# Optimization experiments

Measured on AMD Instinct MI355X. Metric: run time of the kernel, lower is better.

The kernel has to match this reference:

```python
import jax, jax.numpy as jnp
import numpy as np

B, N, H, W, C = 512, 16, 84, 84, 3
CNN_OUT, ATTN, GH, HEADS, POS, A_DIM = 256, 64, 128, 2, 3, 3
IN_GAT = CNN_OUT + POS  # 259
FLAT = 64 * 16 * 16     # conv output flat dim for 84x84 input


def setup_inputs() -> dict:
    key = jax.random.key(0)
    ks = jax.random.split(key, 16)
    s = 0.05
    return dict(
        cam=jax.random.uniform(ks[0], (B, H, W, C), jnp.float32),
        pos=jax.random.normal(ks[1], (B, POS), jnp.float32),
        team_pos=jax.random.normal(ks[2], (B, N, POS), jnp.float32) * 10.0,
        agent_idx=jax.random.randint(ks[3], (B,), 0, N),
        W1=jax.random.normal(ks[4], (32, C, 8, 8), jnp.float32) * s, b1=jnp.zeros((32,), jnp.float32),
        W2=jax.random.normal(ks[5], (64, 32, 4, 4), jnp.float32) * s, b2=jnp.zeros((64,), jnp.float32),
        W3=jax.random.normal(ks[6], (64, 64, 3, 3), jnp.float32) * s, b3=jnp.zeros((64,), jnp.float32),
        Wp=jax.random.normal(ks[7], (FLAT, CNN_OUT), jnp.float32) * 0.01, bp=jnp.zeros((CNN_OUT,), jnp.float32),
        Wid=jax.random.normal(ks[8], (1, ATTN), jnp.float32) * s, bid=jnp.zeros((ATTN,), jnp.float32),
        Wg=jax.random.normal(ks[9], (IN_GAT, HEADS * GH), jnp.float32) * s,
        a_src=jax.random.normal(ks[10], (HEADS, GH), jnp.float32) * s,
        a_dst=jax.random.normal(ks[11], (HEADS, GH), jnp.float32) * s,
        Wh1=jax.random.normal(ks[12], (HEADS * GH + ATTN, 256), jnp.float32) * s, bh1=jnp.zeros((256,), jnp.float32),
        Wh2=jax.random.normal(ks[13], (256, 2 * A_DIM), jnp.float32) * s, bh2=jnp.zeros((2 * A_DIM,), jnp.float32),
    )


def _conv(x, w, b, stride):
    y = jax.lax.conv_general_dilated(x, w, (stride, stride), 'VALID',
                                     dimension_numbers=('NCHW', 'OIHW', 'NCHW'))
    return jax.nn.relu(y + b[None, :, None, None])


def reference(cam, pos, team_pos, agent_idx, W1, b1, W2, b2, W3, b3, Wp, bp,
              Wid, bid, Wg, a_src, a_dst, Wh1, bh1, Wh2, bh2):
    # CNN encoder (NHWC -> NCHW)
    x = jnp.transpose(cam, (0, 3, 1, 2))
    x = _conv(x, W1, b1, 2)   # [B,32,39,39]
    x = _conv(x, W2, b2, 2)   # [B,64,18,18]
    x = _conv(x, W3, b3, 1)   # [B,64,16,16]
    cam_feat = jax.nn.relu(x.reshape(x.shape[0], -1) @ Wp + bp)  # [B,256]

    # per-node features: broadcast ego cam feat + relative team positions
    rel_pos = team_pos - pos[:, None, :]                                     # [B,N,3]
    node_feats = jnp.concatenate(
        [jnp.broadcast_to(cam_feat[:, None, :], (B, N, CNN_OUT)), rel_pos], axis=-1)  # [B,N,259]

    # adjacency: within 100m, no self-loops, self-loop added for isolated nodes
    dist = jnp.linalg.norm(team_pos[:, :, None, :] - team_pos[:, None, :, :], axis=-1)  # [B,N,N]
    eye = jnp.eye(N, dtype=node_feats.dtype)
    adj = (dist < 100.0).astype(node_feats.dtype) * (1.0 - eye)
    need_self = (adj.sum(axis=2) == 0).astype(adj.dtype)                     # [B,N]
    adj = adj + eye[None] * need_self[..., None]

    # dense multi-head GAT layer
    hN = (node_feats @ Wg).reshape(B, N, HEADS, GH)                          # [B,N,H,D]
    src = jnp.einsum('bnhd,hd->bnh', hN, a_src)
    dst = jnp.einsum('bnhd,hd->bnh', hN, a_dst)
    e = jax.nn.leaky_relu(src[:, :, None, :] + dst[:, None, :, :], 0.2)      # [B,i,j,H]
    e = jnp.where(adj[..., None] > 0, e, -1e9)
    alpha = jax.nn.softmax(e, axis=2)
    h = jnp.einsum('bijh,bjhd->bihd', alpha, hN).reshape(B, N, HEADS * GH)   # [B,N,256]
    h = jax.nn.elu(h)
    h = jnp.nan_to_num(h, nan=0.0, posinf=0.0, neginf=0.0)

    # agent-id embedding, fuse, gather own node, policy head
    id_emb = jax.nn.relu(agent_idx.astype(jnp.float32)[:, None] @ Wid + bid)  # [B,64]
    fused = jnp.concatenate([h, jnp.broadcast_to(id_emb[:, None, :], (B, N, ATTN))], axis=-1)  # [B,N,320]
    agent_feat = fused[jnp.arange(B), agent_idx]                             # [B,320]
    z = jax.nn.relu(agent_feat @ Wh1 + bh1)
    logits = z @ Wh2 + bh2                                                    # [B,6]
    return logits
```

## Files before the change

### kernel.cpp

```cpp
#include <hip/hip_runtime.h>


typedef __attribute__((ext_vector_type(8))) short bf16x8;
typedef __attribute__((ext_vector_type(4))) float f32x4;

union U4 { uint4 v; unsigned int u[4]; bf16x8 h; };

__device__ __forceinline__ unsigned short f2bf(float x) {
    unsigned int u = __float_as_uint(x);
    return (unsigned short)((u + 0x7FFFu + ((u >> 16) & 1u)) >> 16);
}
__device__ __forceinline__ unsigned int pack2(float lo, float hi) {
    return (unsigned int)f2bf(lo) | ((unsigned int)f2bf(hi) << 16);
}
__device__ __forceinline__ bf16x8 loadA(const unsigned int* __restrict__ W, int k8, int M, int oc) {
    U4 r; r.v = *(const uint4*)(W + (((size_t)k8 * M + oc) << 2));
    return r.h;
}
__device__ __forceinline__ bf16x8 loadB4(const unsigned int* __restrict__ base, size_t idx) {
    U4 r; r.v = *(const uint4*)(base + (idx << 2));
    return r.h;
}
__device__ __forceinline__ bf16x8 loadBp(const unsigned int* __restrict__ p, size_t BC) {
    U4 r; r.u[0] = p[0]; r.u[1] = p[BC]; r.u[2] = p[2 * BC]; r.u[3] = p[3 * BC];
    return r.h;
}
#define MFMA(a, b, c) __builtin_amdgcn_mfma_f32_16x16x32_bf16((a), (b), (c), 0, 0, 0)

__device__ __forceinline__ int xcd_swz(int L, int nwg) {
    int q = nwg >> 3, r = nwg & 7;
    int x = L & 7, i = L >> 3;
    return (x < r ? x * (q + 1) : r * (q + 1) + (x - r) * q) + i;
}

__device__ __forceinline__ void storeK(unsigned int* __restrict__ out,
                                       size_t row, size_t BC, size_t bcol,
                                       int lg, unsigned int u0, unsigned int u1) {
    uint2 v; v.x = u0; v.y = u1;
    *(uint2*)(out + ((row * BC + bcol) << 2) + ((lg & 1) << 1)) = v;
}

__global__ __launch_bounds__(256) void prepack(
    const float* __restrict__ W1, const float* __restrict__ W2,
    const float* __restrict__ W3, const float* __restrict__ Wp,
    const float* __restrict__ Wg, const float* __restrict__ Wh1,
    unsigned int* __restrict__ W1t, unsigned int* __restrict__ W2t,
    unsigned int* __restrict__ W3t, unsigned int* __restrict__ Wpt,
    unsigned int* __restrict__ Wgt, unsigned int* __restrict__ Wh1t)
{
    int i = blockIdx.x * 256 + threadIdx.x;
    if (i < 3072) {
        int j2 = i & 3, oc = (i >> 2) & 31, k8 = i >> 7;
        int c = k8 >> 3, kh = k8 & 7, kw = 2 * j2;
        const float* s = W1 + ((oc * 3 + c) * 8 + kh) * 8;
        W1t[i] = pack2(s[kw], s[kw + 1]);
    } else if (i < 19456) {
        int j = i - 3072;
        int j2 = j & 3, oc = (j >> 2) & 63, k8 = j >> 8;
        int tap = k8 >> 2, ic = (k8 & 3) * 8 + 2 * j2;
        int kh = tap >> 2, kw = tap & 3;
        float a = W2[((oc * 32 + ic) * 4 + kh) * 4 + kw];
        float b = W2[((oc * 32 + ic + 1) * 4 + kh) * 4 + kw];
        W2t[j] = pack2(a, b);
    } else if (i < 37888) {
        int j = i - 19456;
        int j2 = j & 3, oc = (j >> 2) & 63, k8 = j >> 8;
        int tap = k8 >> 3, ic = (k8 & 7) * 8 + 2 * j2;
        int kh = tap / 3, kw = tap % 3;
        float a = W3[((oc * 64 + ic) * 3 + kh) * 3 + kw];
        float b = W3[((oc * 64 + ic + 1) * 3 + kh) * 3 + kw];
        W3t[j] = pack2(a, b);
    } else if (i < 2135040) {
        int j = i - 37888;
        int j2 = j & 3, n = (j >> 2) & 255, k8 = j >> 10;
        int s3 = k8 >> 3, oc = (k8 & 7) * 8 + 2 * j2;
        float a = Wp[(size_t)(oc * 256 + s3) * 256 + n];
        float b = Wp[(size_t)((oc + 1) * 256 + s3) * 256 + n];
        Wpt[j] = pack2(a, b);
    } else if (i < 2167808) {
        int j = i - 2135040;
        int j2 = j & 3, m = (j >> 2) & 255, k8 = j >> 10;
        int k = k8 * 8 + 2 * j2;
        Wgt[j] = pack2(Wg[k * 256 + m], Wg[(k + 1) * 256 + m]);
    } else if (i < 2208768) {
        int j = i - 2167808;
        int j2 = j & 3, m = (j >> 2) & 255, k8 = j >> 10;
        int k = k8 * 8 + 2 * j2;
        Wh1t[j] = pack2(Wh1[k * 256 + m], Wh1[(k + 1) * 256 + m]);
    }
}

__global__ __launch_bounds__(256) void transpose_cam(
    const float* __restrict__ cam, unsigned int* __restrict__ camt, int b0, int BC)
{
    __shared__ float lds[32][253];
    int yy = blockIdx.x;
    int bb = blockIdx.y * 32;
    int t = threadIdx.x;
    for (int f = t; f < 8064; f += 256) {
        int b = f / 252, p = f - b * 252;
        lds[b][p] = cam[(size_t)(b0 + bb + b) * 21168 + yy * 252 + p];
    }
    __syncthreads();
    for (int g = t; g < 4032; g += 256) {
        int b = g & 31, q = g >> 5;
        int c = q / 42, x2 = q - c * 42;
        unsigned int v = pack2(lds[b][6 * x2 + c], lds[b][6 * x2 + 3 + c]);
        camt[(size_t)((c * 84 + yy) * 42 + x2) * BC + bb + b] = v;
    }
}

__global__ __launch_bounds__(256) void conv1_mfma(
    const unsigned int* __restrict__ in32, const unsigned int* __restrict__ Wt,
    const float* __restrict__ bias, unsigned int* __restrict__ out32,
    int BC, int nspat)
{
    int wgid = xcd_swz(blockIdx.x, gridDim.x);
    int s = wgid % nspat;
    int bq = wgid / nspat;
    int oh = s / 39, ow = s - oh * 39;
    int wv = threadIdx.x >> 6, l = threadIdx.x & 63;
    int lg = l >> 4, lc = l & 15;
    const size_t sBC = (size_t)BC;
    size_t base = (size_t)bq * 256 + wv * 64 + lc;
    f32x4 acc[2][4] = {};
    int ybase = 2 * oh;
    #pragma unroll
    for (int sp = 0; sp < 3; sp++) {
        const int s0 = 2 * sp, s1 = s0 + 1;
        bf16x8 A0[2], A1[2], B0[4], B1[4];
        #pragma unroll
        for (int m = 0; m < 2; m++) {
            A0[m] = loadA(Wt, s0 * 4 + lg, 32, m * 16 + lc);
            A1[m] = loadA(Wt, s1 * 4 + lg, 32, m * 16 + lc);
        }
        const unsigned int* p0 = in32 + (size_t)((sp * 84 + ybase + lg) * 42 + ow) * sBC + base;
        const unsigned int* p1 = in32 + (size_t)((sp * 84 + ybase + 4 + lg) * 42 + ow) * sBC + base;
        #pragma unroll
        for (int g = 0; g < 4; g++) {
            B0[g] = loadBp(p0 + g * 16, sBC);
            B1[g] = loadBp(p1 + g * 16, sBC);
        }
        #pragma unroll
        for (int m = 0; m < 2; m++)
            #pragma unroll
            for (int g = 0; g < 4; g++)
                acc[m][g] = MFMA(A0[m], B0[g], acc[m][g]);
        #pragma unroll
        for (int m = 0; m < 2; m++)
            #pragma unroll
            for (int g = 0; g < 4; g++)
                acc[m][g] = MFMA(A1[m], B1[g], acc[m][g]);
    }
    #pragma unroll
    for (int m = 0; m < 2; m++) {
        float4 bv = *(const float4*)(bias + m * 16 + lg * 4);
        size_t row = (size_t)s * 4 + 2 * m + (lg >> 1);
        #pragma unroll
        for (int g = 0; g < 4; g++) {
            f32x4 a = acc[m][g];
            unsigned int u0 = pack2(fmaxf(a.x + bv.x, 0.f), fmaxf(a.y + bv.y, 0.f));
            unsigned int u1 = pack2(fmaxf(a.z + bv.z, 0.f), fmaxf(a.w + bv.w, 0.f));
            storeK(out32, row, sBC, base + g * 16, lg, u0, u1);
        }
    }
}

__global__ __launch_bounds__(256) void conv2_mfma(
    const unsigned int* __restrict__ in32, const unsigned int* __restrict__ Wt,
    const float* __restrict__ bias, unsigned int* __restrict__ out32,
    int BC, int nspat)
{
    int wgid = xcd_swz(blockIdx.x, gridDim.x);
    int s = wgid % nspat;
    int bq = wgid / nspat;
    int oh = s / 18, ow = s - oh * 18;
    int wv = threadIdx.x >> 6, l = threadIdx.x & 63;
    int lg = l >> 4, lc = l & 15;
    const size_t sBC = (size_t)BC;
    size_t base = (size_t)bq * 256 + wv * 64 + lc;
    f32x4 acc[4][4] = {};
    int ybase = 2 * oh, xbase = 2 * ow;
    #pragma unroll
    for (int sp = 0; sp < 8; sp++) {
        const int s0 = 2 * sp, s1 = s0 + 1;
        bf16x8 A0[4], A1[4], B0[4], B1[4];
        #pragma unroll
        for (int m = 0; m < 4; m++) {
            A0[m] = loadA(Wt, s0 * 4 + lg, 64, m * 16 + lc);
            A1[m] = loadA(Wt, s1 * 4 + lg, 64, m * 16 + lc);
        }
        {
            const int kh = s0 >> 2, kw = s0 & 3;
            size_t row = (size_t)(((ybase + kh) * 39 + xbase + kw) * 4 + lg);
            #pragma unroll
            for (int g = 0; g < 4; g++)
                B0[g] = loadB4(in32, row * sBC + base + g * 16);
        }
        {
            const int kh = s1 >> 2, kw = s1 & 3;
            size_t row = (size_t)(((ybase + kh) * 39 + xbase + kw) * 4 + lg);
            #pragma unroll
            for (int g = 0; g < 4; g++)
                B1[g] = loadB4(in32, row * sBC + base + g * 16);
        }
        #pragma unroll
        for (int m = 0; m < 4; m++)
            #pragma unroll
            for (int g = 0; g < 4; g++)
                acc[m][g] = MFMA(A0[m], B0[g], acc[m][g]);
        #pragma unroll
        for (int m = 0; m < 4; m++)
            #pragma unroll
            for (int g = 0; g < 4; g++)
                acc[m][g] = MFMA(A1[m], B1[g], acc[m][g]);
    }
    #pragma unroll
    for (int m = 0; m < 4; m++) {
        float4 bv = *(const float4*)(bias + m * 16 + lg * 4);
        size_t row = (size_t)s * 8 + 2 * m + (lg >> 1);
        #pragma unroll
        for (int g = 0; g < 4; g++) {
            f32x4 a = acc[m][g];
            unsigned int u0 = pack2(fmaxf(a.x + bv.x, 0.f), fmaxf(a.y + bv.y, 0.f));
            unsigned int u1 = pack2(fmaxf(a.z + bv.z, 0.f), fmaxf(a.w + bv.w, 0.f));
            storeK(out32, row, sBC, base + g * 16, lg, u0, u1);
        }
    }
}

__global__ __launch_bounds__(256) void conv3_mfma(
    const unsigned int* __restrict__ in32, const unsigned int* __restrict__ Wt,
    const float* __restrict__ bias, unsigned int* __restrict__ out32,
    int BC, int nspat)
{
    int wgid = xcd_swz(blockIdx.x, gridDim.x);
    int s = wgid % nspat;
    int bq = wgid / nspat;
    int oh = s >> 4, ow = s & 15;
    int wv = threadIdx.x >> 6, l = threadIdx.x & 63;
    int lg = l >> 4, lc = l & 15;
    const size_t sBC = (size_t)BC;
    size_t base = (size_t)bq * 256 + wv * 64 + lc;
    f32x4 acc[4][4] = {};
    #pragma unroll
    for (int sp = 0; sp < 9; sp++) {
        const int s0 = 2 * sp, s1 = s0 + 1;
        const int kh = sp / 3, kw = sp - kh * 3;
        bf16x8 A0[4], A1[4], B0[4], B1[4];
        #pragma unroll
        for (int m = 0; m < 4; m++) {
            A0[m] = loadA(Wt, s0 * 4 + lg, 64, m * 16 + lc);
            A1[m] = loadA(Wt, s1 * 4 + lg, 64, m * 16 + lc);
        }
        size_t row0 = (size_t)(((oh + kh) * 18 + ow + kw) * 8 + lg);
        #pragma unroll
        for (int g = 0; g < 4; g++) {
            B0[g] = loadB4(in32, row0 * sBC + base + g * 16);
            B1[g] = loadB4(in32, (row0 + 4) * sBC + base + g * 16);
        }
        #pragma unroll
        for (int m = 0; m < 4; m++)
            #pragma unroll
            for (int g = 0; g < 4; g++)
                acc[m][g] = MFMA(A0[m], B0[g], acc[m][g]);
        #pragma unroll
        for (int m = 0; m < 4; m++)
            #pragma unroll
            for (int g = 0; g < 4; g++)
                acc[m][g] = MFMA(A1[m], B1[g], acc[m][g]);
    }
    #pragma unroll
    for (int m = 0; m < 4; m++) {
        float4 bv = *(const float4*)(bias + m * 16 + lg * 4);
        size_t row = (size_t)s * 8 + 2 * m + (lg >> 1);
        #pragma unroll
        for (int g = 0; g < 4; g++) {
            f32x4 a = acc[m][g];
            unsigned int u0 = pack2(fmaxf(a.x + bv.x, 0.f), fmaxf(a.y + bv.y, 0.f));
            unsigned int u1 = pack2(fmaxf(a.z + bv.z, 0.f), fmaxf(a.w + bv.w, 0.f));
            storeK(out32, row, sBC, base + g * 16, lg, u0, u1);
        }
    }
}

__global__ __launch_bounds__(256) void proj_mfma(
    const unsigned int* __restrict__ x3, const unsigned int* __restrict__ Wpt,
    float* __restrict__ partial, int BC)
{
    int wgid = xcd_swz(blockIdx.x, gridDim.x);
    int rem = wgid & 127;
    int bq = wgid >> 7;
    int mq = rem & 3;
    int kseg = rem >> 2;
    int wv = threadIdx.x >> 6, l = threadIdx.x & 63;
    int lg = l >> 4, lc = l & 15;
    const size_t sBC = (size_t)BC;
    size_t base = (size_t)bq * 256 + wv * 64 + lc;
    f32x4 acc[4][4] = {};
    #pragma unroll
    for (int sp = 0; sp < 8; sp++) {
        const int k8b = kseg * 64 + sp * 8;
        bf16x8 A0[4], A1[4], B0[4], B1[4];
        #pragma unroll
        for (int m = 0; m < 4; m++) {
            A0[m] = loadA(Wpt, k8b + lg, 256, mq * 64 + m * 16 + lc);
            A1[m] = loadA(Wpt, k8b + 4 + lg, 256, mq * 64 + m * 16 + lc);
        }
        #pragma unroll
        for (int g = 0; g < 4; g++) {
            B0[g] = loadB4(x3, (size_t)(k8b + lg) * sBC + base + g * 16);
            B1[g] = loadB4(x3, (size_t)(k8b + 4 + lg) * sBC + base + g * 16);
        }
        #pragma unroll
        for (int m = 0; m < 4; m++)
            #pragma unroll
            for (int g = 0; g < 4; g++)
                acc[m][g] = MFMA(A0[m], B0[g], acc[m][g]);
        #pragma unroll
        for (int m = 0; m < 4; m++)
            #pragma unroll
            for (int g = 0; g < 4; g++)
                acc[m][g] = MFMA(A1[m], B1[g], acc[m][g]);
    }
    #pragma unroll
    for (int m = 0; m < 4; m++) {
        size_t row4 = (size_t)kseg * 64 + mq * 16 + m * 4 + lg;
        #pragma unroll
        for (int g = 0; g < 4; g++)
            *(f32x4*)(partial + ((row4 * sBC + base + g * 16) << 2)) = acc[m][g];
    }
}

__global__ __launch_bounds__(256) void reduce_k(
    const float* __restrict__ partial, const float* __restrict__ bp,
    unsigned int* __restrict__ cf16, int b0, int BC, int bcShift)
{
    int i = blockIdx.x * 256 + threadIdx.x;
    int bl = i & (BC - 1);
    int k8 = i >> bcShift;
    f32x4 S0 = {}, S1 = {};
    for (int seg = 0; seg < 32; seg++) {
        const float* p = partial + (((size_t)(seg * 64 + k8 * 2) * BC + bl) << 2);
        S0 += *(const f32x4*)p;
        S1 += *(const f32x4*)(p + (BC << 2));
    }
    int n = k8 * 8;
    uint4 u;
    u.x = pack2(fmaxf(S0.x + bp[n + 0], 0.f), fmaxf(S0.y + bp[n + 1], 0.f));
    u.y = pack2(fmaxf(S0.z + bp[n + 2], 0.f), fmaxf(S0.w + bp[n + 3], 0.f));
    u.z = pack2(fmaxf(S1.x + bp[n + 4], 0.f), fmaxf(S1.y + bp[n + 5], 0.f));
    u.w = pack2(fmaxf(S1.z + bp[n + 6], 0.f), fmaxf(S1.w + bp[n + 7], 0.f));
    *(uint4*)(cf16 + (((size_t)k8 * 512 + b0 + bl) << 2)) = u;
}

__global__ __launch_bounds__(64) void gat_prep(
    const unsigned int* __restrict__ cf16, const unsigned int* __restrict__ Wgt,
    float* __restrict__ hNb)
{
    int mq = blockIdx.x, bq = blockIdx.y;
    int l = threadIdx.x, lg = l >> 4, lc = l & 15;
    size_t bcol = (size_t)bq * 32 + lc;
    f32x4 acc[4][2] = {};
    #pragma unroll
    for (int sp = 0; sp < 4; sp++) {
        const int s0 = 2 * sp, s1 = s0 + 1;
        bf16x8 A0[4], A1[4], B0[2], B1[2];
        #pragma unroll
        for (int m = 0; m < 4; m++) {
            A0[m] = loadA(Wgt, s0 * 4 + lg, 256, mq * 64 + m * 16 + lc);
            A1[m] = loadA(Wgt, s1 * 4 + lg, 256, mq * 64 + m * 16 + lc);
        }
        #pragma unroll
        for (int g = 0; g < 2; g++) {
            B0[g] = loadB4(cf16, (size_t)(s0 * 4 + lg) * 512 + bcol + g * 16);
            B1[g] = loadB4(cf16, (size_t)(s1 * 4 + lg) * 512 + bcol + g * 16);
        }
        #pragma unroll
        for (int m = 0; m < 4; m++) {
            acc[m][0] = MFMA(A0[m], B0[0], acc[m][0]);
            acc[m][1] = MFMA(A0[m], B0[1], acc[m][1]);
            acc[m][0] = MFMA(A1[m], B1[0], acc[m][0]);
            acc[m][1] = MFMA(A1[m], B1[1], acc[m][1]);
        }
    }
    #pragma unroll
    for (int m = 0; m < 4; m++) {
        #pragma unroll
        for (int g = 0; g < 2; g++) {
            size_t b = (size_t)bq * 32 + g * 16 + lc;
            int row0 = mq * 64 + m * 16 + lg * 4;
            *(f32x4*)(hNb + b * 256 + row0) = acc[m][g];
        }
    }
}

__global__ __launch_bounds__(256) void gat_mid(
    const float* __restrict__ hNb, const float* __restrict__ pos,
    const float* __restrict__ tpos, const int* __restrict__ aidx,
    const float* __restrict__ Wg, const float* __restrict__ asrc, const float* __restrict__ adst,
    const float* __restrict__ Wid, const float* __restrict__ bid,
    unsigned int* __restrict__ af16)
{
    int b = blockIdx.x, t = threadIdx.x;
    __shared__ float hN[16][256];
    __shared__ float srcv[16][2], dstv[16][2];
    __shared__ float alpha[16][2];
    __shared__ float af[320];
    __shared__ unsigned int adjm_s;

    int ai = aidx[b];
    float basev = hNb[(size_t)b * 256 + t];
    float rw0 = Wg[65536 + t], rw1 = Wg[65792 + t], rw2 = Wg[66048 + t];
    float px = pos[b * 3 + 0], py = pos[b * 3 + 1], pz = pos[b * 3 + 2];
    for (int n = 0; n < 16; n++) {
        float r0 = tpos[(b * 16 + n) * 3 + 0] - px;
        float r1 = tpos[(b * 16 + n) * 3 + 1] - py;
        float r2 = tpos[(b * 16 + n) * 3 + 2] - pz;
        hN[n][t] = basev + r0 * rw0 + r1 * rw1 + r2 * rw2;
    }

    if (t < 64) {
        bool on = false;
        if (t < 16 && t != ai) {
            float dx = tpos[(b * 16 + ai) * 3 + 0] - tpos[(b * 16 + t) * 3 + 0];
            float dy = tpos[(b * 16 + ai) * 3 + 1] - tpos[(b * 16 + t) * 3 + 1];
            float dz = tpos[(b * 16 + ai) * 3 + 2] - tpos[(b * 16 + t) * 3 + 2];
            on = (dx * dx + dy * dy + dz * dz) < 10000.0f;
        }
        unsigned long long m = __ballot(on);
        if (t == 0) adjm_s = (m == 0ull) ? (1u << ai) : (unsigned int)m;
    }
    __syncthreads();

    {
        int p = t >> 3, sub = t & 7;
        int j = p >> 1, h = p & 1;
        float s1 = 0.f, s2 = 0.f;
        #pragma unroll
        for (int dd = 0; dd < 16; dd++) {
            int d = h * 128 + sub * 16 + dd;
            float v = hN[j][d];
            s1 += v * asrc[d];
            s2 += v * adst[d];
        }
        s1 += __shfl_xor(s1, 1); s1 += __shfl_xor(s1, 2); s1 += __shfl_xor(s1, 4);
        s2 += __shfl_xor(s2, 1); s2 += __shfl_xor(s2, 2); s2 += __shfl_xor(s2, 4);
        if (sub == 0) { srcv[j][h] = s1; dstv[j][h] = s2; }
    }
    __syncthreads();

    if (t < 32) {
        int j = t & 15, h = t >> 4;
        unsigned int am = adjm_s;
        float e = srcv[ai][h] + dstv[j][h];
        e = (e > 0.f) ? e : 0.2f * e;
        e = ((am >> j) & 1u) ? e : -1e9f;
        float mx = e;
        mx = fmaxf(mx, __shfl_xor(mx, 1));
        mx = fmaxf(mx, __shfl_xor(mx, 2));
        mx = fmaxf(mx, __shfl_xor(mx, 4));
        mx = fmaxf(mx, __shfl_xor(mx, 8));
        float ex = __expf(e - mx);
        float sm = ex;
        sm += __shfl_xor(sm, 1); sm += __shfl_xor(sm, 2);
        sm += __shfl_xor(sm, 4); sm += __shfl_xor(sm, 8);
        alpha[j][h] = ex / sm;
    }
    __syncthreads();

    {
        int h = t >> 7;
        float o = 0.f;
        #pragma unroll
        for (int j = 0; j < 16; j++) o += alpha[j][h] * hN[j][t];
        o = (o > 0.f) ? o : (__expf(o) - 1.f);
        af[t] = o;
    }
    if (t < 64) {
        float v = (float)ai * Wid[t] + bid[t];
        af[256 + t] = fmaxf(v, 0.f);
    }
    __syncthreads();

    if (t < 40) {
        uint4 u;
        u.x = pack2(af[t * 8 + 0], af[t * 8 + 1]);
        u.y = pack2(af[t * 8 + 2], af[t * 8 + 3]);
        u.z = pack2(af[t * 8 + 4], af[t * 8 + 5]);
        u.w = pack2(af[t * 8 + 6], af[t * 8 + 7]);
        *(uint4*)(af16 + (((size_t)t * 512 + b) << 2)) = u;
    }
}

__global__ __launch_bounds__(64) void head_mfma(
    const unsigned int* __restrict__ af16, const unsigned int* __restrict__ Wh1t,
    const float* __restrict__ bh1, float* __restrict__ zf)
{
    int mq = blockIdx.x, bq = blockIdx.y;
    int l = threadIdx.x, lg = l >> 4, lc = l & 15;
    size_t bcol = (size_t)bq * 32 + lc;
    f32x4 acc[4][2] = {};
    #pragma unroll
    for (int sp = 0; sp < 5; sp++) {
        const int s0 = 2 * sp, s1 = s0 + 1;
        bf16x8 A0[4], A1[4], B0[2], B1[2];
        #pragma unroll
        for (int m = 0; m < 4; m++) {
            A0[m] = loadA(Wh1t, s0 * 4 + lg, 256, mq * 64 + m * 16 + lc);
            A1[m] = loadA(Wh1t, s1 * 4 + lg, 256, mq * 64 + m * 16 + lc);
        }
        #pragma unroll
        for (int g = 0; g < 2; g++) {
            B0[g] = loadB4(af16, (size_t)(s0 * 4 + lg) * 512 + bcol + g * 16);
            B1[g] = loadB4(af16, (size_t)(s1 * 4 + lg) * 512 + bcol + g * 16);
        }
        #pragma unroll
        for (int m = 0; m < 4; m++) {
            acc[m][0] = MFMA(A0[m], B0[0], acc[m][0]);
            acc[m][1] = MFMA(A0[m], B0[1], acc[m][1]);
            acc[m][0] = MFMA(A1[m], B1[0], acc[m][0]);
            acc[m][1] = MFMA(A1[m], B1[1], acc[m][1]);
        }
    }
    #pragma unroll
    for (int m = 0; m < 4; m++) {
        int row0 = mq * 64 + m * 16 + lg * 4;
        float4 bv = *(const float4*)(bh1 + row0);
        #pragma unroll
        for (int g = 0; g < 2; g++) {
            f32x4 a = acc[m][g];
            size_t b = (size_t)bq * 32 + g * 16 + lc;
            float* pp = zf + (size_t)row0 * 512 + b;
            pp[0]       = fmaxf(a.x + bv.x, 0.f);
            pp[512]     = fmaxf(a.y + bv.y, 0.f);
            pp[2 * 512] = fmaxf(a.z + bv.z, 0.f);
            pp[3 * 512] = fmaxf(a.w + bv.w, 0.f);
        }
    }
}

__global__ __launch_bounds__(256) void logits_k(
    const float* __restrict__ zf, const float* __restrict__ Wh2,
    const float* __restrict__ bh2, float* __restrict__ out)
{
    __shared__ float Ws[1536];
    int t = threadIdx.x;
    int b = blockIdx.x * 256 + t;
    for (int f = t; f < 1536; f += 256) Ws[f] = Wh2[f];
    __syncthreads();
    float acc[6];
    #pragma unroll
    for (int j = 0; j < 6; j++) acc[j] = bh2[j];
    for (int k = 0; k < 256; k++) {
        float zv = zf[(size_t)k * 512 + b];
        #pragma unroll
        for (int j = 0; j < 6; j++) acc[j] += zv * Ws[k * 6 + j];
    }
    #pragma unroll
    for (int j = 0; j < 6; j++) out[b * 6 + j] = acc[j];
}

extern "C" void kernel_launch(void* const* d_in, const int* in_sizes, int n_in,
                              void* d_out, int out_size, void* d_ws, size_t ws_size,
                              hipStream_t stream)
{
    const float* cam  = (const float*)d_in[0];
    const float* pos  = (const float*)d_in[1];
    const float* tpos = (const float*)d_in[2];
    const int*   aidx = (const int*)d_in[3];
    const float* W1   = (const float*)d_in[4];
    const float* b1   = (const float*)d_in[5];
    const float* W2   = (const float*)d_in[6];
    const float* b2   = (const float*)d_in[7];
    const float* W3   = (const float*)d_in[8];
    const float* b3   = (const float*)d_in[9];
    const float* Wp   = (const float*)d_in[10];
    const float* bp   = (const float*)d_in[11];
    const float* Wid  = (const float*)d_in[12];
    const float* bid  = (const float*)d_in[13];
    const float* Wg   = (const float*)d_in[14];
    const float* asrc = (const float*)d_in[15];
    const float* adst = (const float*)d_in[16];
    const float* Wh1  = (const float*)d_in[17];
    const float* bh1  = (const float*)d_in[18];
    const float* Wh2  = (const float*)d_in[19];
    const float* bh2  = (const float*)d_in[20];
    float* out = (float*)d_out;

    int BC = 256;
    if (((size_t)51304 * 512 + 2618368) * 4 <= ws_size) BC = 512;
    int bcShift = (BC == 512) ? 9 : 8;
    int nbq2 = BC >> 8;

    unsigned int* ws32 = (unsigned int*)d_ws;
    unsigned int* RA  = ws32;
    unsigned int* RB  = RA + (size_t)10584 * BC;
    unsigned int* RC  = RB + (size_t)24336 * BC;
    float*        RD  = (float*)(RC + (size_t)8192 * BC);
    unsigned int* W1t = (unsigned int*)(RD + (size_t)8192 * BC);
    unsigned int* W2t  = W1t + 3072;
    unsigned int* W3t  = W2t + 16384;
    unsigned int* Wpt  = W3t + 18432;
    unsigned int* Wgt  = Wpt + 2097152;
    unsigned int* Wh1t = Wgt + 32768;
    unsigned int* cf16 = Wh1t + 40960;
    float*        hNb  = (float*)(cf16 + 65536);
    unsigned int* af16 = (unsigned int*)(hNb + 131072);
    float*        zf   = (float*)(af16 + 81920);

    prepack<<<8628, 256, 0, stream>>>(W1, W2, W3, Wp, Wg, Wh1,
                                      W1t, W2t, W3t, Wpt, Wgt, Wh1t);

    for (int b0 = 0; b0 < 512; b0 += BC) {
        transpose_cam<<<dim3(84, BC / 32), 256, 0, stream>>>(cam, RA, b0, BC);
        conv1_mfma<<<1521 * nbq2, 256, 0, stream>>>(RA, W1t, b1, RB, BC, 1521);
        conv2_mfma<<<324 * nbq2, 256, 0, stream>>>(RB, W2t, b2, RA, BC, 324);
        conv3_mfma<<<256 * nbq2, 256, 0, stream>>>(RA, W3t, b3, RC, BC, 256);
        proj_mfma<<<128 * nbq2, 256, 0, stream>>>(RC, Wpt, RD, BC);
        reduce_k<<<(32 * BC) / 256, 256, 0, stream>>>(RD, bp, cf16, b0, BC, bcShift);
    }
    gat_prep<<<dim3(4, 16), 64, 0, stream>>>(cf16, Wgt, hNb);
    gat_mid<<<512, 256, 0, stream>>>(hNb, pos, tpos, aidx, Wg, asrc, adst,
                                     Wid, bid, af16);
    head_mfma<<<dim3(4, 16), 64, 0, stream>>>(af16, Wh1t, bh1, zf);
    logits_k<<<2, 256, 0, stream>>>(zf, Wh2, bh2, out);
}
```

Before: 147.6 us.

## Repack camera input into channel-padded pixel-pair layout for vectorized conv1 loads

Changes the transposed camera layout so each batch column stores an 8-element bf16 vector holding two adjacent pixels with three channels each, padded with zero to four. conv1 then loads B fragments as single 16-byte loads over 8 K-steps instead of four strided 4-byte loads. W1 is repacked to match, with zero weights in the padded channel slots. This replaces scattered 32-bit gathers with wide coalesced loads, at the cost of a third more cam buffer memory and MFMA work spent on padding zeros.

Measured after the change: 149.3 us. Within noise of the previous version (+1.1%).

```diff
diff --git a/kernel.cpp b/kernel.cpp
--- a/kernel.cpp
+++ b/kernel.cpp
@@ -19,10 +19,6 @@
 }
 __device__ __forceinline__ bf16x8 loadB4(const unsigned int* __restrict__ base, size_t idx) {
     U4 r; r.v = *(const uint4*)(base + (idx << 2));
-    return r.h;
-}
-__device__ __forceinline__ bf16x8 loadBp(const unsigned int* __restrict__ p, size_t BC) {
-    U4 r; r.u[0] = p[0]; r.u[1] = p[BC]; r.u[2] = p[2 * BC]; r.u[3] = p[3 * BC];
     return r.h;
 }
 #define MFMA(a, b, c) __builtin_amdgcn_mfma_f32_16x16x32_bf16((a), (b), (c), 0, 0, 0)
@@ -49,41 +45,48 @@
     unsigned int* __restrict__ Wgt, unsigned int* __restrict__ Wh1t)
 {
     int i = blockIdx.x * 256 + threadIdx.x;
-    if (i < 3072) {
+    if (i < 4096) {
         int j2 = i & 3, oc = (i >> 2) & 31, k8 = i >> 7;
-        int c = k8 >> 3, kh = k8 & 7, kw = 2 * j2;
-        const float* s = W1 + ((oc * 3 + c) * 8 + kh) * 8;
-        W1t[i] = pack2(s[kw], s[kw + 1]);
-    } else if (i < 19456) {
-        int j = i - 3072;
+        int kh = k8 >> 2, kwp = k8 & 3;
+        float w[2];
+        #pragma unroll
+        for (int e = 0; e < 2; e++) {
+            int jj = 2 * j2 + e;
+            int kwlo = jj >> 2, c = jj & 3;
+            w[e] = (c == 3) ? 0.f
+                 : W1[((oc * 3 + c) * 8 + kh) * 8 + 2 * kwp + kwlo];
+        }
+        W1t[i] = pack2(w[0], w[1]);
+    } else if (i < 20480) {
+        int j = i - 4096;
         int j2 = j & 3, oc = (j >> 2) & 63, k8 = j >> 8;
         int tap = k8 >> 2, ic = (k8 & 3) * 8 + 2 * j2;
         int kh = tap >> 2, kw = tap & 3;
         float a = W2[((oc * 32 + ic) * 4 + kh) * 4 + kw];
         float b = W2[((oc * 32 + ic + 1) * 4 + kh) * 4 + kw];
         W2t[j] = pack2(a, b);
-    } else if (i < 37888) {
-        int j = i - 19456;
+    } else if (i < 38912) {
+        int j = i - 20480;
         int j2 = j & 3, oc = (j >> 2) & 63, k8 = j >> 8;
         int tap = k8 >> 3, ic = (k8 & 7) * 8 + 2 * j2;
         int kh = tap / 3, kw = tap % 3;
         float a = W3[((oc * 64 + ic) * 3 + kh) * 3 + kw];
         float b = W3[((oc * 64 + ic + 1) * 3 + kh) * 3 + kw];
         W3t[j] = pack2(a, b);
-    } else if (i < 2135040) {
-        int j = i - 37888;
+    } else if (i < 2136064) {
+        int j = i - 38912;
         int j2 = j & 3, n = (j >> 2) & 255, k8 = j >> 10;
         int s3 = k8 >> 3, oc = (k8 & 7) * 8 + 2 * j2;
         float a = Wp[(size_t)(oc * 256 + s3) * 256 + n];
         float b = Wp[(size_t)((oc + 1) * 256 + s3) * 256 + n];
         Wpt[j] = pack2(a, b);
-    } else if (i < 2167808) {
-        int j = i - 2135040;
+    } else if (i < 2168832) {
+        int j = i - 2136064;
         int j2 = j & 3, m = (j >> 2) & 255, k8 = j >> 10;
         int k = k8 * 8 + 2 * j2;
         Wgt[j] = pack2(Wg[k * 256 + m], Wg[(k + 1) * 256 + m]);
-    } else if (i < 2208768) {
-        int j = i - 2167808;
+    } else if (i < 2209792) {
+        int j = i - 2168832;
         int j2 = j & 3, m = (j >> 2) & 255, k8 = j >> 10;
         int k = k8 * 8 + 2 * j2;
         Wh1t[j] = pack2(Wh1[k * 256 + m], Wh1[(k + 1) * 256 + m]);
@@ -91,7 +94,7 @@
 }
 
 __global__ __launch_bounds__(256) void transpose_cam(
-    const float* __restrict__ cam, unsigned int* __restrict__ camt, int b0, int BC)
+    const float* __restrict__ cam, unsigned int* __restrict__ camq, int b0, int BC)
 {
     __shared__ float lds[32][253];
     int yy = blockIdx.x;
@@ -102,11 +105,15 @@
         lds[b][p] = cam[(size_t)(b0 + bb + b) * 21168 + yy * 252 + p];
     }
     __syncthreads();
-    for (int g = t; g < 4032; g += 256) {
-        int b = g & 31, q = g >> 5;
-        int c = q / 42, x2 = q - c * 42;
-        unsigned int v = pack2(lds[b][6 * x2 + c], lds[b][6 * x2 + 3 + c]);
-        camt[(size_t)((c * 84 + yy) * 42 + x2) * BC + bb + b] = v;
+    for (int g = t; g < 1344; g += 256) {
+        int b = g & 31, xp = g >> 5;
+        const float* l = &lds[b][6 * xp];
+        uint4 u;
+        u.x = pack2(l[0], l[1]);
+        u.y = pack2(l[2], 0.f);
+        u.z = pack2(l[3], l[4]);
+        u.w = pack2(l[5], 0.f);
+        *(uint4*)(camq + (((size_t)(yy * 42 + xp) * BC + bb + b) << 2)) = u;
     }
 }
 
@@ -124,33 +131,20 @@
     const size_t sBC = (size_t)BC;
     size_t base = (size_t)bq * 256 + wv * 64 + lc;
     f32x4 acc[2][4] = {};
-    int ybase = 2 * oh;
-    #pragma unroll
-    for (int sp = 0; sp < 3; sp++) {
-        const int s0 = 2 * sp, s1 = s0 + 1;
-        bf16x8 A0[2], A1[2], B0[4], B1[4];
-        #pragma unroll
-        for (int m = 0; m < 2; m++) {
-            A0[m] = loadA(Wt, s0 * 4 + lg, 32, m * 16 + lc);
-            A1[m] = loadA(Wt, s1 * 4 + lg, 32, m * 16 + lc);
-        }
-        const unsigned int* p0 = in32 + (size_t)((sp * 84 + ybase + lg) * 42 + ow) * sBC + base;
-        const unsigned int* p1 = in32 + (size_t)((sp * 84 + ybase + 4 + lg) * 42 + ow) * sBC + base;
-        #pragma unroll
-        for (int g = 0; g < 4; g++) {
-            B0[g] = loadBp(p0 + g * 16, sBC);
-            B1[g] = loadBp(p1 + g * 16, sBC);
-        }
+    #pragma unroll
+    for (int step = 0; step < 8; step++) {
+        bf16x8 A[2], B[4];
+        A[0] = loadA(Wt, step * 4 + lg, 32, lc);
+        A[1] = loadA(Wt, step * 4 + lg, 32, 16 + lc);
+        size_t row = (size_t)((2 * oh + step) * 42 + ow + lg);
+        #pragma unroll
+        for (int g = 0; g < 4; g++)
+            B[g] = loadB4(in32, row * sBC + base + g * 16);
         #pragma unroll
         for (int m = 0; m < 2; m++)
             #pragma unroll
             for (int g = 0; g < 4; g++)
-                acc[m][g] = MFMA(A0[m], B0[g], acc[m][g]);
-        #pragma unroll
-        for (int m = 0; m < 2; m++)
-            #pragma unroll
-            for (int g = 0; g < 4; g++)
-                acc[m][g] = MFMA(A1[m], B1[g], acc[m][g]);
+                acc[m][g] = MFMA(A[m], B[g], acc[m][g]);
     }
     #pragma unroll
     for (int m = 0; m < 2; m++) {
@@ -589,17 +583,17 @@
     float* out = (float*)d_out;
 
     int BC = 256;
-    if (((size_t)51304 * 512 + 2618368) * 4 <= ws_size) BC = 512;
+    if (((size_t)54832 * 512 + 2619392) * 4 <= ws_size) BC = 512;
     int bcShift = (BC == 512) ? 9 : 8;
     int nbq2 = BC >> 8;
 
     unsigned int* ws32 = (unsigned int*)d_ws;
     unsigned int* RA  = ws32;
-    unsigned int* RB  = RA + (size_t)10584 * BC;
+    unsigned int* RB  = RA + (size_t)14112 * BC;
     unsigned int* RC  = RB + (size_t)24336 * BC;
     float*        RD  = (float*)(RC + (size_t)8192 * BC);
     unsigned int* W1t = (unsigned int*)(RD + (size_t)8192 * BC);
-    unsigned int* W2t  = W1t + 3072;
+    unsigned int* W2t  = W1t + 4096;
     unsigned int* W3t  = W2t + 16384;
     unsigned int* Wpt  = W3t + 18432;
     unsigned int* Wgt  = Wpt + 2097152;
@@ -609,7 +603,7 @@
     unsigned int* af16 = (unsigned int*)(hNb + 131072);
     float*        zf   = (float*)(af16 + 81920);
 
-    prepack<<<8628, 256, 0, stream>>>(W1, W2, W3, Wp, Wg, Wh1,
+    prepack<<<8632, 256, 0, stream>>>(W1, W2, W3, Wp, Wg, Wh1,
                                       W1t, W2t, W3t, Wpt, Wgt, Wh1t);
 
     for (int b0 = 0; b0 < 512; b0 += BC) {
```
